# Kernel optimization log

Measured on AMD Instinct MI355X. Metric: run time of the kernel, lower is better.

The kernel has to match this reference:

```python
import jax, jax.numpy as jnp
import numpy as np

N_SRC = 1024     # source frames
N_TGT = 100000   # target pool frames
D = 1024         # WavLM layer-6 feature dim
K = 4            # neighbors


def setup_inputs() -> dict:
    key = jax.random.key(0)
    k1, k2 = jax.random.split(key)
    source_feats = jax.random.normal(k1, (N_SRC, D), dtype=jnp.float32)
    target_feats = jax.random.normal(k2, (N_TGT, D), dtype=jnp.float32)
    return {"source_feats": source_feats, "target_feats": target_feats, "k": K}


def reference(source_feats, target_feats, k):
    # Cosine distance kNN: smallest cosine distance == largest cosine similarity.
    s = source_feats / jnp.linalg.norm(source_feats, axis=-1, keepdims=True)
    t = target_feats / jnp.linalg.norm(target_feats, axis=-1, keepdims=True)
    sim = jnp.einsum('nd,md->nm', s, t)          # [N_SRC, N_TGT]
    _, idx = jax.lax.top_k(sim, k)               # [N_SRC, k] neighbor indices
    # Gather ORIGINAL (un-normalized) target rows and average over neighbors,
    # matching sklearn kneighbors + target_np[indices].mean(axis=0).
    gathered = target_feats[idx]                 # [N_SRC, k, D]
    return gathered.mean(axis=1)                 # [N_SRC, D]
```

## Files before the change

### kernel.cpp

```cpp
#include <hip/hip_runtime.h>
#include <hip/hip_bf16.h>
#include <float.h>

#define N_SRC 1024
#define N_TGT 100000
#define DIM   1024
#define KNN   4

#define BM 128
#define BN 256
#define BK 64
#define NKT (DIM / BK)
#define NMB 782
#define N_TGT2 (NMB * BM)
#define NSC (N_SRC / BN)
#define NBLK (NMB * NSC)
#define NSTRIP NMB
#define NCAND (NSTRIP * KNN)
#define RERANK 32

#define SRC_KT_B 65536ull
#define TGT_KT_B ((unsigned long long)N_TGT2 * 64ull)

typedef __attribute__((ext_vector_type(4))) float f32x4;
typedef __attribute__((ext_vector_type(4))) unsigned int u32x4;
typedef __attribute__((ext_vector_type(2))) long long i64x2;

__device__ __forceinline__ void gload16(const void* gp, void* lp) {
    __builtin_amdgcn_global_load_lds(
        (const __attribute__((address_space(1))) void*)gp,
        (__attribute__((address_space(3))) void*)lp, 16, 0, 0);
}

__device__ __forceinline__ unsigned int pk_fp8x4(float x0, float x1,
                                                 float x2, float x3) {
    int d = __builtin_amdgcn_cvt_pk_fp8_f32(x0, x1, 0, false);
    d     = __builtin_amdgcn_cvt_pk_fp8_f32(x2, x3, d, true);
    return (unsigned int)d;
}

__device__ __forceinline__ void ce_desc(float& v1, int& i1, float& v2, int& i2)
{
    bool sw = (v2 > v1) || (v2 == v1 && i2 < i1);
    float tv = sw ? v2 : v1; float uv = sw ? v1 : v2;
    int   ti = sw ? i2 : i1; int   ui = sw ? i1 : i2;
    v1 = tv; i1 = ti; v2 = uv; i2 = ui;
}

__global__ __launch_bounds__(256) void convert_src_kernel(
    const float* __restrict__ src, unsigned int* __restrict__ srcws)
{
    int gid = blockIdx.x * 256 + threadIdx.x;
    int kt  = gid >> 12;
    int rem = gid & 4095;
    int row = rem >> 2;
    int pos = rem & 3;
    int c   = pos ^ ((row >> 1) & 3);
    const float4* p0 = (const float4*)(src + (size_t)row * DIM + kt * BK + c * 8);
    const float4* p1 = (const float4*)(src + (size_t)row * DIM + kt * BK + 32 + c * 8);
    float4 a0 = p0[0], a1 = p0[1], b0 = p1[0], b1 = p1[1];
    u32x4 o = { pk_fp8x4(a0.x, a0.y, a0.z, a0.w),
                pk_fp8x4(a1.x, a1.y, a1.z, a1.w),
                pk_fp8x4(b0.x, b0.y, b0.z, b0.w),
                pk_fp8x4(b1.x, b1.y, b1.z, b1.w) };
    ((u32x4*)srcws)[gid] = o;
}

__global__ __launch_bounds__(256) void prep_tgt_kernel(
    const float* __restrict__ tgt, unsigned int* __restrict__ tgtbf,
    float* __restrict__ invnw)
{
    __shared__ float pn[16][17];
    const int t  = threadIdx.x;
    const int li = t & 15;
    const int kt = t >> 4;
    const int row = blockIdx.x * 16 + li;
    const bool valid = row < N_TGT;

    float4 v[16];
    if (valid) {
        const float4* p = (const float4*)(tgt + (size_t)row * DIM + kt * BK);
        #pragma unroll
        for (int i = 0; i < 16; ++i) v[i] = p[i];
    } else {
        #pragma unroll
        for (int i = 0; i < 16; ++i) v[i] = make_float4(0.f, 0.f, 0.f, 0.f);
    }
    float nsq = 0.f;
    #pragma unroll
    for (int i = 0; i < 16; ++i)
        nsq += v[i].x * v[i].x + v[i].y * v[i].y
             + v[i].z * v[i].z + v[i].w * v[i].w;

    u32x4* o = (u32x4*)((char*)tgtbf + (size_t)kt * TGT_KT_B
                        + (size_t)row * 64);
    const int f = (row >> 1) & 3;
    #pragma unroll
    for (int c = 0; c < 4; ++c) {
        float4 a0 = v[2 * c], a1 = v[2 * c + 1];
        float4 b0 = v[8 + 2 * c], b1 = v[8 + 2 * c + 1];
        o[c ^ f] = (u32x4){ pk_fp8x4(a0.x, a0.y, a0.z, a0.w),
                            pk_fp8x4(a1.x, a1.y, a1.z, a1.w),
                            pk_fp8x4(b0.x, b0.y, b0.z, b0.w),
                            pk_fp8x4(b1.x, b1.y, b1.z, b1.w) };
    }

    pn[li][kt] = nsq;
    __syncthreads();
    if (t < 16) {
        float s = 0.f;
        #pragma unroll
        for (int k = 0; k < 16; ++k) s += pn[t][k];
        int r2 = blockIdx.x * 16 + t;
        invnw[r2] = (r2 < N_TGT) ? 1.0f / sqrtf(s) : -1.0f;
    }
}

__global__ __launch_bounds__(512, 4) void gemm_topk_fp8_kernel(
    const void* __restrict__ tgtbf, const void* __restrict__ srcbf,
    const float* __restrict__ invnw,
    float* __restrict__ cand_val, int* __restrict__ cand_idx)
{
    __shared__ __align__(16) unsigned char As[3][BM][BK];
    __shared__ __align__(16) unsigned char Bs[3][BN][BK];
    __shared__ float invn_sh[BM];

    const int b = blockIdx.x;
    const int logical = (b & 7) * (NBLK / 8) + (b >> 3);
    const int mblk = logical >> 2;
    const int schk = logical & 3;
    const int m0 = mblk * BM;
    const int c0 = schk * BN;

    const int t = threadIdx.x;
    const int lane = t & 63;
    const int w = t >> 6;
    const int wm = w >> 2, wn = w & 3;
    const int g = lane >> 4, li = lane & 15;

    const char* tb_ = (const char*)tgtbf;
    const char* sb_ = (const char*)srcbf;

    f32x4 acc[4][4];
    #pragma unroll
    for (int i = 0; i < 4; ++i)
        #pragma unroll
        for (int j = 0; j < 4; ++j) acc[i][j] = (f32x4){0.f, 0.f, 0.f, 0.f};

    unsigned char *Ac = &As[0][0][0], *An1 = &As[1][0][0], *An2 = &As[2][0][0];
    unsigned char *Bc = &Bs[0][0][0], *Bn1 = &Bs[1][0][0], *Bn2 = &Bs[2][0][0];

    #define STAGE(Ab_, Bb_, kt_) do {                                         \
        const char* ga_ = tb_ + (size_t)(kt_) * TGT_KT_B + (size_t)m0 * 64    \
                          + (size_t)t * 16;                                   \
        gload16(ga_, (Ab_) + t * 16);                                         \
        const char* gb_ = sb_ + (size_t)(kt_) * SRC_KT_B + (size_t)c0 * 64    \
                          + (size_t)t * 16;                                   \
        gload16(gb_,        (Bb_) + t * 16);                                  \
        gload16(gb_ + 8192, (Bb_) + 8192 + t * 16);                           \
    } while (0)

    const int sl = (g ^ ((li >> 1) & 3)) * 16;

    #define READ_AB do {                                                      \
        _Pragma("unroll")                                                     \
        for (int mf = 0; mf < 4; ++mf)                                        \
            af[mf] = *(const i64x2*)(Ac + (wm * 64 + mf * 16 + li) * BK + sl);\
        _Pragma("unroll")                                                     \
        for (int nf = 0; nf < 4; ++nf)                                        \
            bf[nf] = *(const i64x2*)(Bc + (wn * 64 + nf * 16 + li) * BK + sl);\
    } while (0)

    #define DO_MFMA do {                                                      \
        _Pragma("unroll")                                                     \
        for (int mf = 0; mf < 4; ++mf)                                        \
            _Pragma("unroll")                                                 \
            for (int nf = 0; nf < 4; ++nf)                                    \
                acc[mf][nf] = __builtin_amdgcn_mfma_f32_16x16x32_fp8_fp8(     \
                    af[mf][0], bf[nf][0], acc[mf][nf], 0, 0, 0);              \
        _Pragma("unroll")                                                     \
        for (int mf = 0; mf < 4; ++mf)                                        \
            _Pragma("unroll")                                                 \
            for (int nf = 0; nf < 4; ++nf)                                    \
                acc[mf][nf] = __builtin_amdgcn_mfma_f32_16x16x32_fp8_fp8(     \
                    af[mf][1], bf[nf][1], acc[mf][nf], 0, 0, 0);              \
    } while (0)

    #define ROTATE do {                                                       \
        unsigned char* tmp_;                                                  \
        tmp_ = Ac; Ac = An1; An1 = An2; An2 = tmp_;                           \
        tmp_ = Bc; Bc = Bn1; Bn1 = Bn2; Bn2 = tmp_;                           \
    } while (0)

    STAGE(Ac, Bc, 0);
    STAGE(An1, Bn1, 1);
    asm volatile("s_waitcnt vmcnt(3)" ::: "memory");
    __builtin_amdgcn_sched_barrier(0);
    __builtin_amdgcn_s_barrier();

    for (int kt = 0; kt < NKT - 2; ++kt) {
        STAGE(An2, Bn2, kt + 2);
        i64x2 af[4], bf[4];
        READ_AB;
        DO_MFMA;
        asm volatile("s_waitcnt vmcnt(3)" ::: "memory");
        __builtin_amdgcn_sched_barrier(0);
        __builtin_amdgcn_s_barrier();
        ROTATE;
    }
    {
        i64x2 af[4], bf[4];
        READ_AB;
        DO_MFMA;
        asm volatile("s_waitcnt vmcnt(0)" ::: "memory");
        __builtin_amdgcn_sched_barrier(0);
        __builtin_amdgcn_s_barrier();
        ROTATE;
    }
    {
        i64x2 af[4], bf[4];
        READ_AB;
        DO_MFMA;
        __syncthreads();
    }
    #undef STAGE
    #undef READ_AB
    #undef DO_MFMA
    #undef ROTATE

    float* scv = (float*)&As[0][0][0];
    int*   sci = (int*)&As[1][0][0];

    if (t < BM) invn_sh[t] = invnw[m0 + t];
    __syncthreads();

    float invr[4][4];
    #pragma unroll
    for (int mf = 0; mf < 4; ++mf)
        #pragma unroll
        for (int j = 0; j < 4; ++j)
            invr[mf][j] = invn_sh[wm * 64 + mf * 16 + g * 4 + j];

    #pragma unroll
    for (int nf = 0; nf < 4; ++nf) {
        const int col = wn * 64 + nf * 16 + li;
        float s[4][4];
        #pragma unroll
        for (int mf = 0; mf < 4; ++mf)
            #pragma unroll
            for (int j = 0; j < 4; ++j)
                s[mf][j] = (invr[mf][j] > 0.f) ? acc[mf][nf][j] * invr[mf][j]
                                               : -FLT_MAX;
        #pragma unroll
        for (int it = 0; it < KNN; ++it) {
            float bv = -FLT_MAX; int bli = 0;
            #pragma unroll
            for (int mf = 0; mf < 4; ++mf)
                #pragma unroll
                for (int j = 0; j < 4; ++j) {
                    int id = mf * 16 + g * 4 + j;
                    if (s[mf][j] > bv) { bv = s[mf][j]; bli = id; }
                }
            #pragma unroll
            for (int off = 16; off < 64; off <<= 1) {
                float ov = __shfl_xor(bv, off);
                int   oi = __shfl_xor(bli, off);
                if (ov > bv || (ov == bv && oi < bli)) { bv = ov; bli = oi; }
            }
            const int mfw = bli >> 4, gw = (bli >> 2) & 3, jw = bli & 3;
            if (g == gw) {
                #pragma unroll
                for (int mf = 0; mf < 4; ++mf)
                    #pragma unroll
                    for (int j = 0; j < 4; ++j)
                        if (mf == mfw && j == jw) s[mf][j] = -FLT_MAX;
            }
            if (g == it) {
                int o = (wm * BN + col) * KNN + it;
                scv[o] = bv;
                sci[o] = m0 + wm * 64 + bli;
            }
        }
    }
    __syncthreads();

    if (t < BN) {
        float v4[4] = { -FLT_MAX, -FLT_MAX, -FLT_MAX, -FLT_MAX };
        int   i4[4] = { 0x7fffffff, 0x7fffffff, 0x7fffffff, 0x7fffffff };
        #pragma unroll
        for (int q = 0; q < 8; ++q) {
            int o = ((q >> 2) * BN + t) * KNN + (q & 3);
            float v = scv[o]; int ix = sci[o];
            if (v > v4[3] || (v == v4[3] && ix < i4[3])) {
                v4[3] = v; i4[3] = ix;
                ce_desc(v4[2], i4[2], v4[3], i4[3]);
                ce_desc(v4[1], i4[1], v4[2], i4[2]);
                ce_desc(v4[0], i4[0], v4[1], i4[1]);
            }
        }
        size_t o = ((size_t)(c0 + t) * NSTRIP + mblk) * KNN;
        #pragma unroll
        for (int it = 0; it < KNN; ++it) {
            cand_val[o + it] = v4[it];
            cand_idx[o + it] = i4[it];
        }
    }
}

__global__ __launch_bounds__(256) void merge_rerank_kernel(
    const float* __restrict__ src, const float* __restrict__ tgt,
    const float* __restrict__ cand_val, const int* __restrict__ cand_idx,
    float* __restrict__ out)
{
    __shared__ float sv[NCAND];
    __shared__ float red_v[4];
    __shared__ int   red_p[4];
    __shared__ int   topi[RERANK];
    __shared__ float rsim[RERANK];
    __shared__ int   ridx[RERANK];
    __shared__ int   sel[KNN];

    const int row = blockIdx.x;
    const int t = threadIdx.x, lane = t & 63, w = t >> 6;
    const float* cv = cand_val + (size_t)row * NCAND;
    const int*   ci = cand_idx + (size_t)row * NCAND;

    for (int i = t; i < NCAND; i += 256) sv[i] = cv[i];
    __syncthreads();

    for (int it = 0; it < RERANK; ++it) {
        float bv = -FLT_MAX; int bp = 0;
        for (int i = t; i < NCAND; i += 256) {
            float v = sv[i];
            if (v > bv) { bv = v; bp = i; }
        }
        #pragma unroll
        for (int off = 1; off < 64; off <<= 1) {
            float ov = __shfl_xor(bv, off);
            int   op = __shfl_xor(bp, off);
            if (ov > bv || (ov == bv && op < bp)) { bv = ov; bp = op; }
        }
        if (lane == 0) { red_v[w] = bv; red_p[w] = bp; }
        __syncthreads();
        if (t == 0) {
            float Bv = red_v[0]; int Bp = red_p[0];
            for (int q = 1; q < 4; ++q)
                if (red_v[q] > Bv || (red_v[q] == Bv && red_p[q] < Bp)) {
                    Bv = red_v[q]; Bp = red_p[q];
                }
            topi[it] = ci[Bp];
            sv[Bp] = -FLT_MAX;
        }
        __syncthreads();
    }

    const float4* sp = (const float4*)(src + (size_t)row * DIM);
    #pragma unroll
    for (int q = 0; q < 8; ++q) {
        int cidx = topi[w + 4 * q];
        const float4* tp = (const float4*)(tgt + (size_t)cidx * DIM);
        float a = 0.f, nn = 0.f;
        #pragma unroll
        for (int p = 0; p < 4; ++p) {
            float4 x = sp[lane + 64 * p], y = tp[lane + 64 * p];
            a  = fmaf(x.x, y.x, a);  a  = fmaf(x.y, y.y, a);
            a  = fmaf(x.z, y.z, a);  a  = fmaf(x.w, y.w, a);
            nn = fmaf(y.x, y.x, nn); nn = fmaf(y.y, y.y, nn);
            nn = fmaf(y.z, y.z, nn); nn = fmaf(y.w, y.w, nn);
        }
        #pragma unroll
        for (int off = 1; off < 64; off <<= 1) {
            a  += __shfl_xor(a, off);
            nn += __shfl_xor(nn, off);
        }
        if (lane == 0) { rsim[w + 4 * q] = a / sqrtf(nn); ridx[w + 4 * q] = cidx; }
    }
    __syncthreads();

    if (w == 0) {
        float v = (lane < RERANK) ? rsim[lane] : -FLT_MAX;
        int  ix = (lane < RERANK) ? ridx[lane] : 0x7fffffff;
        #pragma unroll
        for (int it = 0; it < KNN; ++it) {
            float bv = v; int bix = ix;
            #pragma unroll
            for (int off = 1; off < 32; off <<= 1) {
                float ov = __shfl_xor(bv, off);
                int   oi = __shfl_xor(bix, off);
                if (ov > bv || (ov == bv && oi < bix)) { bv = ov; bix = oi; }
            }
            if (lane == 0) sel[it] = bix;
            if (ix == bix) v = -FLT_MAX;
        }
    }
    __syncthreads();

    const float4* g0 = (const float4*)(tgt + (size_t)sel[0] * DIM);
    const float4* g1 = (const float4*)(tgt + (size_t)sel[1] * DIM);
    const float4* g2 = (const float4*)(tgt + (size_t)sel[2] * DIM);
    const float4* g3 = (const float4*)(tgt + (size_t)sel[3] * DIM);
    float4* po = (float4*)(out + (size_t)row * DIM);
    float4 v0 = g0[t], v1 = g1[t], v2 = g2[t], v3 = g3[t];
    float4 rr;
    rr.x = (v0.x + v1.x + v2.x + v3.x) * 0.25f;
    rr.y = (v0.y + v1.y + v2.y + v3.y) * 0.25f;
    rr.z = (v0.z + v1.z + v2.z + v3.z) * 0.25f;
    rr.w = (v0.w + v1.w + v2.w + v3.w) * 0.25f;
    po[t] = rr;
}

extern "C" void kernel_launch(void* const* d_in, const int* in_sizes, int n_in,
                              void* d_out, int out_size, void* d_ws, size_t ws_size,
                              hipStream_t stream)
{
    const float* src = (const float*)d_in[0];
    const float* tgt = (const float*)d_in[1];
    float* out = (float*)d_out;

    const size_t SRCBF_B = 2097152;
    const size_t TGTBF_B = (size_t)N_TGT2 * 1024;
    const size_t INVN_B  = (size_t)N_TGT2 * 4;
    const size_t CV_B    = (size_t)N_SRC * NCAND * 4;

    char* p = (char*)d_ws;
    unsigned int* srcbf = (unsigned int*)p;
    unsigned int* tgtbf = (unsigned int*)(p + SRCBF_B);
    float* invnw    = (float*)(p + SRCBF_B + TGTBF_B);
    float* cand_val = (float*)(p + SRCBF_B + TGTBF_B + INVN_B);
    int*   cand_idx = (int*)(p + SRCBF_B + TGTBF_B + INVN_B + CV_B);

    convert_src_kernel<<<256, 256, 0, stream>>>(src, srcbf);
    prep_tgt_kernel<<<N_TGT2 / 16, 256, 0, stream>>>(tgt, tgtbf, invnw);
    gemm_topk_fp8_kernel<<<NBLK, 512, 0, stream>>>(tgtbf, srcbf, invnw,
                                                   cand_val, cand_idx);
    merge_rerank_kernel<<<N_SRC, 256, 0, stream>>>(src, tgt,
                                                   cand_val, cand_idx, out);
}
```

Baseline: 387.9 us.

## Split GEMM k-step into two phases with barriers and MFMA priority

Splits each k-tile iteration into two half-phases, interleaving the LDS reads and global loads with MFMA clusters over N-fragment pairs. Each MFMA phase is fenced by workgroup barriers and raised wave priority (s_setprio) to get ping-pong style overlap of memory and matrix work across waves. This adds extra barriers per k-step, which may cost more than the overlap it gains.

New measurement: 374.1 us, median of 2. -3.5%, faster.

```diff
diff --git a/kernel.cpp b/kernel.cpp
--- a/kernel.cpp
+++ b/kernel.cpp
@@ -150,82 +150,127 @@
     unsigned char *Ac = &As[0][0][0], *An1 = &As[1][0][0], *An2 = &As[2][0][0];
     unsigned char *Bc = &Bs[0][0][0], *Bn1 = &Bs[1][0][0], *Bn2 = &Bs[2][0][0];
 
-    #define STAGE(Ab_, Bb_, kt_) do {                                         \
-        const char* ga_ = tb_ + (size_t)(kt_) * TGT_KT_B + (size_t)m0 * 64    \
-                          + (size_t)t * 16;                                   \
-        gload16(ga_, (Ab_) + t * 16);                                         \
-        const char* gb_ = sb_ + (size_t)(kt_) * SRC_KT_B + (size_t)c0 * 64    \
-                          + (size_t)t * 16;                                   \
-        gload16(gb_,        (Bb_) + t * 16);                                  \
-        gload16(gb_ + 8192, (Bb_) + 8192 + t * 16);                           \
+    #define STAGE_A(Ab_, kt_) do {                                            \
+        gload16(tb_ + (size_t)(kt_) * TGT_KT_B + (size_t)m0 * 64              \
+                + (size_t)t * 16, (Ab_) + t * 16);                            \
+    } while (0)
+    #define STAGE_B1(Bb_, kt_) do {                                           \
+        gload16(sb_ + (size_t)(kt_) * SRC_KT_B + (size_t)c0 * 64              \
+                + (size_t)t * 16, (Bb_) + t * 16);                            \
+    } while (0)
+    #define STAGE_B2(Bb_, kt_) do {                                           \
+        gload16(sb_ + (size_t)(kt_) * SRC_KT_B + (size_t)c0 * 64 + 8192       \
+                + (size_t)t * 16, (Bb_) + 8192 + t * 16);                     \
     } while (0)
 
     const int sl = (g ^ ((li >> 1) & 3)) * 16;
 
-    #define READ_AB do {                                                      \
+    #define READ_A4 do {                                                      \
         _Pragma("unroll")                                                     \
         for (int mf = 0; mf < 4; ++mf)                                        \
             af[mf] = *(const i64x2*)(Ac + (wm * 64 + mf * 16 + li) * BK + sl);\
-        _Pragma("unroll")                                                     \
-        for (int nf = 0; nf < 4; ++nf)                                        \
-            bf[nf] = *(const i64x2*)(Bc + (wn * 64 + nf * 16 + li) * BK + sl);\
-    } while (0)
-
-    #define DO_MFMA do {                                                      \
+    } while (0)
+    #define READ_B01 do {                                                     \
+        bf[0] = *(const i64x2*)(Bc + (wn * 64 +  0 + li) * BK + sl);          \
+        bf[1] = *(const i64x2*)(Bc + (wn * 64 + 16 + li) * BK + sl);          \
+    } while (0)
+    #define READ_B23 do {                                                     \
+        bf[2] = *(const i64x2*)(Bc + (wn * 64 + 32 + li) * BK + sl);          \
+        bf[3] = *(const i64x2*)(Bc + (wn * 64 + 48 + li) * BK + sl);          \
+    } while (0)
+
+    #define MFMA_NPAIR(n0_) do {                                              \
         _Pragma("unroll")                                                     \
         for (int mf = 0; mf < 4; ++mf)                                        \
             _Pragma("unroll")                                                 \
-            for (int nf = 0; nf < 4; ++nf)                                    \
+            for (int nf = (n0_); nf < (n0_) + 2; ++nf)                        \
                 acc[mf][nf] = __builtin_amdgcn_mfma_f32_16x16x32_fp8_fp8(     \
                     af[mf][0], bf[nf][0], acc[mf][nf], 0, 0, 0);              \
         _Pragma("unroll")                                                     \
         for (int mf = 0; mf < 4; ++mf)                                        \
             _Pragma("unroll")                                                 \
-            for (int nf = 0; nf < 4; ++nf)                                    \
+            for (int nf = (n0_); nf < (n0_) + 2; ++nf)                        \
                 acc[mf][nf] = __builtin_amdgcn_mfma_f32_16x16x32_fp8_fp8(     \
                     af[mf][1], bf[nf][1], acc[mf][nf], 0, 0, 0);              \
     } while (0)
 
+    #define PH_ENTER do {                                                     \
+        __builtin_amdgcn_s_barrier();                                         \
+        asm volatile("s_waitcnt lgkmcnt(0)" ::: "memory");                    \
+        __builtin_amdgcn_sched_barrier(0);                                    \
+        __builtin_amdgcn_s_setprio(1);                                        \
+    } while (0)
+    #define PH_EXIT do {                                                      \
+        __builtin_amdgcn_s_setprio(0);                                        \
+        __builtin_amdgcn_s_barrier();                                         \
+    } while (0)
     #define ROTATE do {                                                       \
         unsigned char* tmp_;                                                  \
         tmp_ = Ac; Ac = An1; An1 = An2; An2 = tmp_;                           \
         tmp_ = Bc; Bc = Bn1; Bn1 = Bn2; Bn2 = tmp_;                           \
     } while (0)
 
-    STAGE(Ac, Bc, 0);
-    STAGE(An1, Bn1, 1);
+    STAGE_A(Ac, 0);  STAGE_B1(Bc, 0);  STAGE_B2(Bc, 0);
+    STAGE_A(An1, 1); STAGE_B1(Bn1, 1); STAGE_B2(Bn1, 1);
     asm volatile("s_waitcnt vmcnt(3)" ::: "memory");
     __builtin_amdgcn_sched_barrier(0);
     __builtin_amdgcn_s_barrier();
 
     for (int kt = 0; kt < NKT - 2; ++kt) {
-        STAGE(An2, Bn2, kt + 2);
         i64x2 af[4], bf[4];
-        READ_AB;
-        DO_MFMA;
+        READ_A4;
+        READ_B01;
+        STAGE_A(An2, kt + 2);
+        STAGE_B1(Bn2, kt + 2);
+        PH_ENTER;
+        MFMA_NPAIR(0);
+        PH_EXIT;
+        READ_B23;
+        STAGE_B2(Bn2, kt + 2);
         asm volatile("s_waitcnt vmcnt(3)" ::: "memory");
         __builtin_amdgcn_sched_barrier(0);
-        __builtin_amdgcn_s_barrier();
+        PH_ENTER;
+        MFMA_NPAIR(2);
+        PH_EXIT;
         ROTATE;
     }
     {
         i64x2 af[4], bf[4];
-        READ_AB;
-        DO_MFMA;
+        READ_A4;
+        READ_B01;
+        PH_ENTER;
+        MFMA_NPAIR(0);
+        PH_EXIT;
+        READ_B23;
         asm volatile("s_waitcnt vmcnt(0)" ::: "memory");
         __builtin_amdgcn_sched_barrier(0);
-        __builtin_amdgcn_s_barrier();
+        PH_ENTER;
+        MFMA_NPAIR(2);
+        PH_EXIT;
         ROTATE;
     }
     {
         i64x2 af[4], bf[4];
-        READ_AB;
-        DO_MFMA;
+        READ_A4;
+        READ_B01;
+        PH_ENTER;
+        MFMA_NPAIR(0);
+        PH_EXIT;
+        READ_B23;
+        PH_ENTER;
+        MFMA_NPAIR(2);
+        PH_EXIT;
         __syncthreads();
     }
-    #undef STAGE
-    #undef READ_AB
-    #undef DO_MFMA
+    #undef STAGE_A
+    #undef STAGE_B1
+    #undef STAGE_B2
+    #undef READ_A4
+    #undef READ_B01
+    #undef READ_B23
+    #undef MFMA_NPAIR
+    #undef PH_ENTER
+    #undef PH_EXIT
     #undef ROTATE
 
     float* scv = (float*)&As[0][0][0];
```
